# Kernel optimization log

Hardware: AMD Instinct MI355X
Metric: run time of the kernel (lower is better)

## Reference

```python
import jax, jax.numpy as jnp
import numpy as np

NUM_CAPSULE = 16
DIM_CAPSULE = 16
NUM_ROUTING = 3
EPS = 1e-7  # K.epsilon()


def squash(v, axis=-1):
    s2 = jnp.sum(jnp.square(v), axis=axis, keepdims=True) + EPS
    scale = s2 / ((1.0 + s2) * jnp.sqrt(s2))
    return scale * v


def setup_inputs() -> dict:
    key = jax.random.key(0)
    k1, k2 = jax.random.split(key)
    B, N, IC, ID = 64, 128, 32, 8
    x = jax.random.normal(k1, (B, N, IC, ID), dtype=jnp.float32)
    # glorot_uniform for W: [IC, ID, NUM_CAPSULE*DIM_CAPSULE]
    fan_in, fan_out = ID, NUM_CAPSULE * DIM_CAPSULE
    limit = np.sqrt(6.0 / (fan_in + fan_out))
    W = jax.random.uniform(k2, (IC, ID, NUM_CAPSULE * DIM_CAPSULE), dtype=jnp.float32,
                           minval=-limit, maxval=limit)
    return {"x": x, "W": W}


def reference(x, W):
    B, N, IC, ID = x.shape
    NC, DC = NUM_CAPSULE, DIM_CAPSULE
    u = x.reshape(-1, IC, ID)  # [BN, IC, ID]
    # prediction vectors: [BN, IC, NC*DC] -> [BN, NC, IC, DC]
    u_hat = jnp.einsum('bij,ijk->bik', u, W).reshape(-1, IC, NC, DC).transpose(0, 2, 1, 3)
    u_hat_stopped = jax.lax.stop_gradient(u_hat)
    b = jnp.zeros((u_hat.shape[0], NC, IC), dtype=x.dtype)
    outputs = None
    for i in range(NUM_ROUTING):
        c = jax.nn.softmax(b, axis=1)  # softmax over num_capsule axis (dim=1 in source)
        hat = u_hat if i == NUM_ROUTING - 1 else u_hat_stopped
        outputs = squash(jnp.einsum('bci,bcid->bcd', c, hat))  # [BN, NC, DC]
        if i < NUM_ROUTING - 1:
            b = b + jnp.einsum('bcd,bcid->bci', outputs, u_hat_stopped)
    return outputs.reshape(B, N, NC, DC)
```

## Files before the change

### kernel.cpp

```cpp
#include <hip/hip_runtime.h>
#include <hip/hip_bf16.h>


#define S 2

typedef float    v2f __attribute__((ext_vector_type(2)));
typedef _Float16 v2h __attribute__((ext_vector_type(2)));

__device__ __forceinline__ v2h pack2h(float a, float b) {
  return __builtin_bit_cast(v2h, __builtin_amdgcn_cvt_pkrtz(a, b));
}

template <int CTRL>
__device__ __forceinline__ float dppf(float x) {
  return __builtin_bit_cast(float,
      __builtin_amdgcn_update_dpp(0, __builtin_bit_cast(int, x), CTRL, 0xF, 0xF, true));
}
template <int CTRL>
__device__ __forceinline__ v2h dpph(v2h v) {
  return __builtin_bit_cast(v2h,
      __builtin_amdgcn_update_dpp(0, __builtin_bit_cast(int, v), CTRL, 0xF, 0xF, true));
}
template <int CTRL, int BANK>
__device__ __forceinline__ int dpp_old_i(int old, int x) {
  return __builtin_amdgcn_update_dpp(old, x, CTRL, 0xF, BANK, false);
}
__device__ __forceinline__ v2h xor4t_h(v2h s) {
  int si = __builtin_bit_cast(int, s);
  int ya = dpp_old_i<0x104, 0x5>(0, si);
  return __builtin_bit_cast(v2h, dpp_old_i<0x114, 0xA>(ya, si));
}

#if __has_builtin(__builtin_amdgcn_fdot2)
__device__ __forceinline__ float dot2(v2h a, v2h b, float c) {
  return __builtin_amdgcn_fdot2(a, b, c, false);
}
#else
__device__ __forceinline__ float dot2(v2h a, v2h b, float c) {
  return fmaf((float)a.x, (float)b.x, fmaf((float)a.y, (float)b.y, c));
}
#endif

__global__ __launch_bounds__(256) void prep_kernel(const float* __restrict__ W,
                                                   const float* __restrict__ x,
                                                   _Float16* __restrict__ Wth,
                                                   _Float16* __restrict__ xh) {
  int bid = blockIdx.x;
  if (bid < 256) {
    int o       = bid * 256 + threadIdx.x;
    int ic_slot = o >> 11;
    int k       = (o >> 3) & 255;
    int id      = o & 7;
    int ic_src  = (ic_slot & 16) | ((ic_slot ^ k) & 15);
    Wth[o] = (_Float16)W[(ic_src * 8 + id) * 256 + k];
  } else {
    int tid = (bid - 256) * 256 + threadIdx.x;
    const float4* xp = (const float4*)x + tid * 2;
    float4 f0 = xp[0], f1 = xp[1];
    v2h h0 = {(_Float16)f0.x, (_Float16)f0.y};
    v2h h1 = {(_Float16)f0.z, (_Float16)f0.w};
    v2h h2 = {(_Float16)f1.x, (_Float16)f1.y};
    v2h h3 = {(_Float16)f1.z, (_Float16)f1.w};
    uint4 o;
    o.x = __builtin_bit_cast(unsigned, h0);
    o.y = __builtin_bit_cast(unsigned, h1);
    o.z = __builtin_bit_cast(unsigned, h2);
    o.w = __builtin_bit_cast(unsigned, h3);
    ((uint4*)xh)[tid] = o;
  }
}

__device__ __forceinline__ v2f squash2(v2f o) {
  v2f s2 = o * o;
  s2.x += dppf<0xB1>(s2.x);   s2.y += dppf<0xB1>(s2.y);
  s2.x += dppf<0x4E>(s2.x);   s2.y += dppf<0x4E>(s2.y);
  s2.x += dppf<0x141>(s2.x);  s2.y += dppf<0x141>(s2.y);
  s2.x += dppf<0x140>(s2.x);  s2.y += dppf<0x140>(s2.y);
  s2 += (v2f){1e-7f, 1e-7f};
  v2f sc;
  sc.x = s2.x * __builtin_amdgcn_rsqf(s2.x) * __builtin_amdgcn_rcpf(1.f + s2.x);
  sc.y = s2.y * __builtin_amdgcn_rsqf(s2.y) * __builtin_amdgcn_rcpf(1.f + s2.y);
  return o * sc;
}

template <bool ASSIGN>
__device__ __forceinline__ void b_update2(v2h vh, const v2h* uhx, int dc,
                                          float* bp0, float* bp1) {
#pragma unroll
  for (int icb = 0; icb < 32; icb += 16) {
    v2h y[16];
#pragma unroll
    for (int j = 0; j < 16; ++j) y[j] = vh * uhx[icb + j];
#pragma unroll
    for (int j = 0; j < 8; ++j) y[j] += dpph<0x128>(y[j + 8]);
#pragma unroll
    for (int j = 0; j < 4; ++j) y[j] += xor4t_h(y[j + 4]);
#pragma unroll
    for (int j = 0; j < 2; ++j) y[j] += dpph<0x4E>(y[j + 2]);
    y[0] += dpph<0xB1>(y[1]);
    float e0 = (float)y[0].x, e1 = (float)y[0].y;
    if (ASSIGN) { bp0[icb + dc] = e0;  bp1[icb + dc] = e1; }
    else        { bp0[icb + dc] += e0; bp1[icb + dc] += e1; }
  }
}

__global__ __launch_bounds__(256, 4) void caps_kernel(const unsigned* __restrict__ xh32,
                                                      const uint4* __restrict__ Wt4,
                                                      float* __restrict__ out) {
  const int t  = threadIdx.x;
  const int nc = t >> 4;
  const int dc = t & 15;
  const int s0 = blockIdx.x * S;

  __shared__ float b_lds[S][16][33];
  __shared__ _Float16 c16h[16][32][2];
  __shared__ __align__(16) _Float16 xh_lds[2 * 256];

  ((unsigned*)xh_lds)[t] = xh32[s0 * 128 + t];
  __syncthreads();

  v2h uhx[32];
  v2f o2 = (v2f){0.f, 0.f};

#pragma unroll
  for (int ic = 0; ic < 32; ++ic) {
    uint4 wv = Wt4[ic * 256 + t];
    v2h w0 = __builtin_bit_cast(v2h, wv.x);
    v2h w1 = __builtin_bit_cast(v2h, wv.y);
    v2h w2 = __builtin_bit_cast(v2h, wv.z);
    v2h w3 = __builtin_bit_cast(v2h, wv.w);
    const int icx0 = (ic & 16) | ((ic ^ dc) & 15);
    uint4 xv0 = *(const uint4*)(xh_lds + icx0 * 8);
    uint4 xv1 = *(const uint4*)(xh_lds + 256 + icx0 * 8);
    float a0 = dot2(__builtin_bit_cast(v2h, xv0.w), w3,
               dot2(__builtin_bit_cast(v2h, xv0.z), w2,
               dot2(__builtin_bit_cast(v2h, xv0.y), w1,
               dot2(__builtin_bit_cast(v2h, xv0.x), w0, 0.f))));
    float a1 = dot2(__builtin_bit_cast(v2h, xv1.w), w3,
               dot2(__builtin_bit_cast(v2h, xv1.z), w2,
               dot2(__builtin_bit_cast(v2h, xv1.y), w1,
               dot2(__builtin_bit_cast(v2h, xv1.x), w0, 0.f))));
    o2 += (v2f){a0, a1};
    uhx[ic] = pack2h(a0, a1);
  }

  {
    v2f v = squash2(o2 * (v2f){0.0625f, 0.0625f});
    v2h vh = pack2h(v.x, v.y);
    b_update2<true>(vh, uhx, dc, &b_lds[0][nc][0], &b_lds[1][nc][0]);
  }
  __syncthreads();

#pragma unroll
  for (int r = 1; r < 3; ++r) {
    {
      const int ss  = t >> 7;
      const int icc = (t >> 2) & 31;
      const int q   = t & 3;
      float e0 = __expf(b_lds[ss][4 * q + 0][icc]);
      float e1 = __expf(b_lds[ss][4 * q + 1][icc]);
      float e2 = __expf(b_lds[ss][4 * q + 2][icc]);
      float e3 = __expf(b_lds[ss][4 * q + 3][icc]);
      float ps = (e0 + e1) + (e2 + e3);
      ps += dppf<0xB1>(ps);
      ps += dppf<0x4E>(ps);
      float inv = __builtin_amdgcn_rcpf(ps);
      c16h[4 * q + 0][icc][ss] = (_Float16)(e0 * inv);
      c16h[4 * q + 1][icc][ss] = (_Float16)(e1 * inv);
      c16h[4 * q + 2][icc][ss] = (_Float16)(e2 * inv);
      c16h[4 * q + 3][icc][ss] = (_Float16)(e3 * inv);
    }
    __syncthreads();

    const v2h* crow = (const v2h*)&c16h[nc][0][0];
    v2h oh = (v2h){(_Float16)0.f, (_Float16)0.f};
#pragma unroll
    for (int j = 0; j < 16; ++j) {
      const int m = j ^ dc;
      v2h cA = crow[m];
      v2h cB = crow[m + 16];
      oh = __builtin_elementwise_fma(cA, uhx[j], oh);
      oh = __builtin_elementwise_fma(cB, uhx[16 + j], oh);
    }
    v2f o = (v2f){(float)oh.x, (float)oh.y};
    v2f v = squash2(o);
    if (r == 2) {
      out[(s0 + 0) * 256 + t] = v.x;
      out[(s0 + 1) * 256 + t] = v.y;
    } else {
      v2h vh = pack2h(v.x, v.y);
      b_update2<false>(vh, uhx, dc, &b_lds[0][nc][0], &b_lds[1][nc][0]);
      __syncthreads();
    }
  }
}

extern "C" void kernel_launch(void* const* d_in, const int* in_sizes, int n_in,
                              void* d_out, int out_size, void* d_ws, size_t ws_size,
                              hipStream_t stream) {
  const float* x = (const float*)d_in[0];
  const float* W = (const float*)d_in[1];
  _Float16* Wth = (_Float16*)d_ws;
  _Float16* xh  = (_Float16*)d_ws + 65536;

  prep_kernel<<<1280, 256, 0, stream>>>(W, x, Wth, xh);
  caps_kernel<<<8192 / S, 256, 0, stream>>>((const unsigned*)xh, (const uint4*)Wth,
                                            (float*)d_out);
}
```

Baseline: 98.51 us.

## Fuse x fp16 conversion into caps kernel and pad softmax coefficient LDS rows

```diff
diff --git a/kernel.cpp b/kernel.cpp
--- a/kernel.cpp
+++ b/kernel.cpp
@@ -42,32 +42,13 @@
 #endif
 
 __global__ __launch_bounds__(256) void prep_kernel(const float* __restrict__ W,
-                                                   const float* __restrict__ x,
-                                                   _Float16* __restrict__ Wth,
-                                                   _Float16* __restrict__ xh) {
-  int bid = blockIdx.x;
-  if (bid < 256) {
-    int o       = bid * 256 + threadIdx.x;
-    int ic_slot = o >> 11;
-    int k       = (o >> 3) & 255;
-    int id      = o & 7;
-    int ic_src  = (ic_slot & 16) | ((ic_slot ^ k) & 15);
-    Wth[o] = (_Float16)W[(ic_src * 8 + id) * 256 + k];
-  } else {
-    int tid = (bid - 256) * 256 + threadIdx.x;
-    const float4* xp = (const float4*)x + tid * 2;
-    float4 f0 = xp[0], f1 = xp[1];
-    v2h h0 = {(_Float16)f0.x, (_Float16)f0.y};
-    v2h h1 = {(_Float16)f0.z, (_Float16)f0.w};
-    v2h h2 = {(_Float16)f1.x, (_Float16)f1.y};
-    v2h h3 = {(_Float16)f1.z, (_Float16)f1.w};
-    uint4 o;
-    o.x = __builtin_bit_cast(unsigned, h0);
-    o.y = __builtin_bit_cast(unsigned, h1);
-    o.z = __builtin_bit_cast(unsigned, h2);
-    o.w = __builtin_bit_cast(unsigned, h3);
-    ((uint4*)xh)[tid] = o;
-  }
+                                                   _Float16* __restrict__ Wth) {
+  int o       = blockIdx.x * 256 + threadIdx.x;
+  int ic_slot = o >> 11;
+  int k       = (o >> 3) & 255;
+  int id      = o & 7;
+  int ic_src  = (ic_slot & 16) | ((ic_slot ^ k) & 15);
+  Wth[o] = (_Float16)W[(ic_src * 8 + id) * 256 + k];
 }
 
 __device__ __forceinline__ v2f squash2(v2f o) {
@@ -104,7 +85,9 @@
   }
 }
 
-__global__ __launch_bounds__(256, 4) void caps_kernel(const unsigned* __restrict__ xh32,
+#define CSTRIDE 40
+
+__global__ __launch_bounds__(256, 4) void caps_kernel(const float* __restrict__ x,
                                                       const uint4* __restrict__ Wt4,
                                                       float* __restrict__ out) {
   const int t  = threadIdx.x;
@@ -113,10 +96,14 @@
   const int s0 = blockIdx.x * S;
 
   __shared__ float b_lds[S][16][33];
-  __shared__ _Float16 c16h[16][32][2];
+  __shared__ v2h c16h[16 * CSTRIDE];
   __shared__ __align__(16) _Float16 xh_lds[2 * 256];
 
-  ((unsigned*)xh_lds)[t] = xh32[s0 * 128 + t];
+  {
+    const float2* xs = (const float2*)(x + s0 * 256);
+    float2 xv = xs[t];
+    ((unsigned*)xh_lds)[t] = __builtin_bit_cast(unsigned, pack2h(xv.x, xv.y));
+  }
   __syncthreads();
 
   v2h uhx[32];
@@ -165,14 +152,15 @@
       ps += dppf<0xB1>(ps);
       ps += dppf<0x4E>(ps);
       float inv = __builtin_amdgcn_rcpf(ps);
-      c16h[4 * q + 0][icc][ss] = (_Float16)(e0 * inv);
-      c16h[4 * q + 1][icc][ss] = (_Float16)(e1 * inv);
-      c16h[4 * q + 2][icc][ss] = (_Float16)(e2 * inv);
-      c16h[4 * q + 3][icc][ss] = (_Float16)(e3 * inv);
+      _Float16* cw = (_Float16*)c16h + ss;
+      cw[((4 * q + 0) * CSTRIDE + icc) * 2] = (_Float16)(e0 * inv);
+      cw[((4 * q + 1) * CSTRIDE + icc) * 2] = (_Float16)(e1 * inv);
+      cw[((4 * q + 2) * CSTRIDE + icc) * 2] = (_Float16)(e2 * inv);
+      cw[((4 * q + 3) * CSTRIDE + icc) * 2] = (_Float16)(e3 * inv);
     }
     __syncthreads();
 
-    const v2h* crow = (const v2h*)&c16h[nc][0][0];
+    const v2h* crow = &c16h[nc * CSTRIDE];
     v2h oh = (v2h){(_Float16)0.f, (_Float16)0.f};
 #pragma unroll
     for (int j = 0; j < 16; ++j) {
@@ -201,9 +189,7 @@
   const float* x = (const float*)d_in[0];
   const float* W = (const float*)d_in[1];
   _Float16* Wth = (_Float16*)d_ws;
-  _Float16* xh  = (_Float16*)d_ws + 65536;
 
-  prep_kernel<<<1280, 256, 0, stream>>>(W, x, Wth, xh);
-  caps_kernel<<<8192 / S, 256, 0, stream>>>((const unsigned*)xh, (const uint4*)Wth,
-                                            (float*)d_out);
+  prep_kernel<<<256, 256, 0, stream>>>(W, Wth);
+  caps_kernel<<<8192 / S, 256, 0, stream>>>(x, (const uint4*)Wth, (float*)d_out);
 }
```

Measured after the change: 97.14 us. No clear change (-1.4%).
